# Performance work log

Hardware: AMD Instinct MI355X
Metric: run time of the kernel (lower is better)

The kernel has to match this reference:

```python
import jax, jax.numpy as jnp
import numpy as np
from jax import lax

B, T, C = 2, 2048, 1024
H, D = 16, 64            # num_heads, head_dim
K = 4                    # short conv kernel size
BASE = 10000.0
MAX_SEQ = 262144.0
ORIG_MAX = 8192.0
SCALING = 32.0
EPS = 1e-6


def _rope_cos_sin(t_len):
    ar = jnp.arange(0, D, 2).astype(jnp.float32) / D           # (D/2,)
    ext = MAX_SEQ / ORIG_MAX
    scaled_base = BASE * ext ** (D / (D - 2))
    inv_freq = 1.0 / scaled_base ** ar                          # (D/2,)
    freq_extra = 1.0 / BASE ** ar
    wavelen = 2 * np.pi / freq_extra
    beta_fast, beta_slow = 1.0, 32.0
    mscale = jnp.clip((wavelen - beta_fast) / (beta_slow - beta_fast), 0.0, 1.0)
    scale = 1.0 + (SCALING - 1.0) * mscale                      # per-freq t scaling
    t = jnp.arange(t_len, dtype=jnp.float32)[:, None] / scale[None, :]
    freqs = t * inv_freq[None, :]                               # (T, D/2)
    emb = jnp.concatenate([freqs, freqs], axis=-1)              # (T, D)
    return jnp.cos(emb), jnp.sin(emb)


def _apply_rotary(x, cos, sin):
    # x: (B,T,H,D); cos/sin: (T,D); faithful to torch interleaved indexing
    ce = cos[None, :, None, ::2]
    se = sin[None, :, None, ::2]
    x1, x2 = x[..., ::2], x[..., 1::2]
    return jnp.concatenate([x1 * ce - x2 * se, x1 * se + x2 * ce], axis=-1)


def _short_conv(x, w, b):
    # causal depthwise conv1d + silu. x: (B,T,C), w: (C,1,K), b: (C,)
    xp = jnp.pad(x, ((0, 0), (K - 1, 0), (0, 0))).transpose(0, 2, 1)  # (B,C,T+K-1)
    y = lax.conv_general_dilated(xp, w, window_strides=(1,), padding='VALID',
                                 feature_group_count=C,
                                 dimension_numbers=('NCH', 'OIH', 'NCH'))
    y = y + b[None, :, None]
    return jax.nn.silu(y.transpose(0, 2, 1))


def _l2norm(x):
    n = jnp.sqrt(jnp.sum(x * x, axis=-1, keepdims=True))
    return x / jnp.maximum(n, 1e-12)


def _rmsnorm(x, w):
    ms = jnp.mean(x.astype(jnp.float32) ** 2, axis=-1, keepdims=True).astype(x.dtype)
    return w * (x * lax.rsqrt(ms + EPS))


def setup_inputs() -> dict:
    key = jax.random.key(0)
    ks = jax.random.split(key, 20)
    s = 0.02
    inp = {
        'x': jax.random.normal(ks[0], (B, T, C), jnp.float32),
        'Wq': jax.random.normal(ks[1], (H * D, C), jnp.float32) * s,
        'Wk': jax.random.normal(ks[2], (H * D, C), jnp.float32) * s,
        'Wv': jax.random.normal(ks[3], (H * D, C), jnp.float32) * s,
        'Wg': jax.random.normal(ks[4], (H * D, C), jnp.float32) * s,
        'Wo': jax.random.normal(ks[5], (C, H * D), jnp.float32) * s,
        'Wb': jax.random.normal(ks[6], (H, C), jnp.float32) * s,
        'bb': jnp.zeros((H,), jnp.float32),
        'Wgk': jax.random.normal(ks[7], (H, C), jnp.float32) * s,
        'bgk': jnp.zeros((H,), jnp.float32),
        'conv_q_w': jax.random.normal(ks[8], (H * D, 1, K), jnp.float32) * 0.1,
        'conv_q_b': jnp.zeros((H * D,), jnp.float32),
        'conv_k_w': jax.random.normal(ks[9], (H * D, 1, K), jnp.float32) * 0.1,
        'conv_k_b': jnp.zeros((H * D,), jnp.float32),
        'conv_v_w': jax.random.normal(ks[10], (H * D, 1, K), jnp.float32) * 0.1,
        'conv_v_b': jnp.zeros((H * D,), jnp.float32),
        'A_log': jnp.log(jax.random.uniform(ks[11], (H,), jnp.float32, 1e-4, 16.0)),
        'Dp': jnp.ones((H,), jnp.float32),
        'dt_bias': jax.random.uniform(ks[12], (H,), jnp.float32, -0.01, 0.01),
        'o_norm_w': jnp.ones((D,), jnp.float32),
    }
    return inp


def reference(x, Wq, Wk, Wv, Wg, Wo, Wb, bb, Wgk, bgk,
              conv_q_w, conv_q_b, conv_k_w, conv_k_b, conv_v_w, conv_v_b,
              A_log, Dp, dt_bias, o_norm_w):
    q = _short_conv(x @ Wq.T, conv_q_w, conv_q_b)
    k = _short_conv(x @ Wk.T, conv_k_w, conv_k_b)
    v = _short_conv(x @ Wv.T, conv_v_w, conv_v_b)
    g = (x @ Wg.T).reshape(B, T, H, D)

    q = q.reshape(B, T, H, D)
    k = k.reshape(B, T, H, D)
    v = v.reshape(B, T, H, D)

    cos, sin = _rope_cos_sin(T)
    q = _l2norm(_apply_rotary(q, cos, sin))
    k = _l2norm(_apply_rotary(k, cos, sin))

    beta = jax.nn.sigmoid(x @ Wb.T + bb)                       # (B,T,H)
    gk = x @ Wgk.T + bgk                                       # (B,T,H)
    A = jnp.exp(A_log)
    alpha = jnp.exp(-A[None, None, :] * jax.nn.softplus(gk + dt_bias))  # (B,T,H)

    # gated delta rule: S_t = alpha_t*(S - beta_t*(S k)k^T) + beta_t*v k^T; o_t = S_t q_t
    def step(S, inp):
        qt, kt, vt, at, bt = inp                               # (B,H,D) x3, (B,H) x2
        Sk = jnp.einsum('bhvk,bhk->bhv', S, kt)
        outer = kt[:, :, None, :]
        S = (at[:, :, None, None] * (S - bt[:, :, None, None] * Sk[..., None] * outer)
             + bt[:, :, None, None] * vt[..., None] * outer)
        o = jnp.einsum('bhvk,bhk->bhv', S, qt)
        return S, o

    tm = lambda a: jnp.swapaxes(a, 0, 1)                        # time-major
    S0 = jnp.zeros((B, H, D, D), x.dtype)
    _, o = lax.scan(step, S0, (tm(q), tm(k), tm(v), tm(alpha), tm(beta)))
    o = jnp.swapaxes(o, 0, 1)                                  # (B,T,H,D)

    o = o + Dp[None, None, :, None] * v                        # D skip connection
    o = g * jax.nn.silu(_rmsnorm(o, o_norm_w))                 # fused RMSNorm-swish gate
    return o.reshape(B, T, H * D) @ Wo.T
```

## Files before the change

### kernel.cpp

```cpp
#include <hip/hip_runtime.h>

#define Bsz 2
#define Tsz 2048
#define Csz 1024
#define Hsz 16
#define Dsz 64
#define BT (Bsz*Tsz)

typedef unsigned short u16;
typedef __attribute__((ext_vector_type(8))) short bf16x8_t;
typedef __attribute__((ext_vector_type(4))) float f32x4;
typedef __attribute__((ext_vector_type(4))) unsigned short us4;

#define MF(a,b,c) __builtin_amdgcn_mfma_f32_16x16x32_bf16(a,b,c,0,0,0)

__device__ __forceinline__ float bf2f(u16 u){
    union { unsigned i; float f; } c; c.i = ((unsigned)u) << 16; return c.f;
}
__device__ __forceinline__ u16 f2bf(float f){
    union { float f; unsigned i; } c; c.f = f;
    unsigned i = c.i;
    unsigned r = (i + 0x7fffu + ((i >> 16) & 1u)) >> 16;
    return (u16)r;
}
__device__ __forceinline__ void gload_lds16(const void* g, void* l){
    __builtin_amdgcn_global_load_lds(
        (const __attribute__((address_space(1))) unsigned int*)g,
        (__attribute__((address_space(3))) unsigned int*)l, 16, 0, 0);
}

__global__ void rope_tables_k(float* __restrict__ ctab, float* __restrict__ stab){
    int idx = blockIdx.x * blockDim.x + threadIdx.x;
    if (idx >= Tsz * 16) return;
    int t = idx >> 4, m = idx & 15;
    float arf = (float)m / 16.f;
    double sb = 10000.0 * pow(32.0, 64.0 / 62.0);
    float invf = (float)(1.0 / pow(sb, (double)arf));
    float fe   = (float)(1.0 / pow(10000.0, (double)arf));
    float wl   = 6.283185307179586f / fe;
    float ms   = fminf(fmaxf((wl - 1.0f) / 31.0f, 0.f), 1.f);
    float scale = 1.f + 31.f * ms;
    float freq = ((float)t / scale) * invf;
    ctab[idx] = cosf(freq);
    stab[idx] = sinf(freq);
}

__global__ void cvt_f32_bf16_k(const float* __restrict__ in, u16* __restrict__ out, int n){
    int i = (blockIdx.x * blockDim.x + threadIdx.x) * 4;
    if (i >= n) return;
    float4 v = *(const float4*)(in + i);
    us4 o; o.x = f2bf(v.x); o.y = f2bf(v.y); o.z = f2bf(v.z); o.w = f2bf(v.w);
    *(us4*)(out + i) = o;
}

__global__ __launch_bounds__(256) void gemm_bf16_nt(
    const u16* __restrict__ A, const u16* __restrict__ Bw,
    float* __restrict__ Cf, u16* __restrict__ Cb,
    int gm, long sstride, int Kdim)
{
    __shared__ u16 As[2][128*32];
    __shared__ u16 Bs[2][128*32];

    const int nwg = gridDim.x;
    const int q8  = nwg >> 3;
    const int id  = blockIdx.x;
    const int swz = (id & 7) * q8 + (id >> 3);
    const int bx  = swz % gm;
    const int by  = swz / gm;

    const int tid = threadIdx.x;
    const int w  = tid >> 6, l = tid & 63;
    const int lm = l & 15,  lg = l >> 4;
    const int wm = (w >> 1) << 6;
    const int wn = (w & 1) << 6;

    const int r0  = (w << 4) + (l >> 2);
    const int kof = (l & 3) * 8;
    const long ga0 = (long)(bx * 128 + r0)      * Kdim + kof;
    const long ga1 = (long)(bx * 128 + r0 + 64) * Kdim + kof;
    const long gb0 = (long)(by * 128 + r0)      * Kdim + kof;
    const long gb1 = (long)(by * 128 + r0 + 64) * Kdim + kof;
    const int  ldst = r0 * 32 + kof;

    f32x4 acc[4][4];
#pragma unroll
    for (int i = 0; i < 4; i++)
#pragma unroll
        for (int j = 0; j < 4; j++) acc[i][j] = (f32x4){0.f, 0.f, 0.f, 0.f};

    const int nt = Kdim >> 5;
#define STAGE(B_, T_) do { int k0_ = (T_) << 5;                       \
        gload_lds16(A  + ga0 + k0_, &As[B_][ldst]);                   \
        gload_lds16(A  + ga1 + k0_, &As[B_][ldst + 2048]);            \
        gload_lds16(Bw + gb0 + k0_, &Bs[B_][ldst]);                   \
        gload_lds16(Bw + gb1 + k0_, &Bs[B_][ldst + 2048]);            \
    } while (0)

    STAGE(0, 0);
    __syncthreads();
    int buf = 0;
    for (int t = 0; t < nt; t++) {
        if (t + 1 < nt) STAGE(buf ^ 1, t + 1);
        bf16x8_t av[4], bv[4];
#pragma unroll
        for (int i = 0; i < 4; i++) av[i] = *(const bf16x8_t*)&As[buf][(wm + i*16 + lm)*32 + lg*8];
#pragma unroll
        for (int j = 0; j < 4; j++) bv[j] = *(const bf16x8_t*)&Bs[buf][(wn + j*16 + lm)*32 + lg*8];
#pragma unroll
        for (int i = 0; i < 4; i++)
#pragma unroll
            for (int j = 0; j < 4; j++)
                acc[i][j] = MF(av[i], bv[j], acc[i][j]);
        __syncthreads();
        buf ^= 1;
    }
#undef STAGE

    const int crow0 = bx * 128 + wm + lg * 4;
    const int ccol0 = by * 128 + wn + lm;
#pragma unroll
    for (int i = 0; i < 4; i++)
#pragma unroll
        for (int j = 0; j < 4; j++)
#pragma unroll
            for (int r = 0; r < 4; r++) {
                long row = crow0 + i * 16 + r;
                int  col = ccol0 + j * 16;
                float vv = acc[i][j][r];
                if (Cf) Cf[row * 1024 + col] = vv;
                else    Cb[(long)(col >> 10) * sstride + row * 1024 + (col & 1023)] = f2bf(vv);
            }
}

__global__ __launch_bounds__(256) void conv_silu_k(
    const u16* __restrict__ pre, const float* __restrict__ w,
    const float* __restrict__ bias, float* __restrict__ out)
{
    int c  = blockIdx.y * 256 + threadIdx.x;
    int bi = blockIdx.x;
    int b  = bi >> 5;
    int t0 = (bi & 31) << 6;
    float w0 = w[c*4+0], w1 = w[c*4+1], w2 = w[c*4+2], w3 = w[c*4+3];
    float bs = bias[c];
    long base = ((long)b * Tsz) * Csz + c;
    float xm3 = (t0 >= 3) ? bf2f(pre[base + (long)(t0-3)*Csz]) : 0.f;
    float xm2 = (t0 >= 2) ? bf2f(pre[base + (long)(t0-2)*Csz]) : 0.f;
    float xm1 = (t0 >= 1) ? bf2f(pre[base + (long)(t0-1)*Csz]) : 0.f;
    for (int t = t0; t < t0 + 64; t++) {
        float xc = bf2f(pre[base + (long)t * Csz]);
        float z  = bs + w0*xm3 + w1*xm2 + w2*xm1 + w3*xc;
        out[base + (long)t * Csz] = z / (1.f + expf(-z));
        xm3 = xm2; xm2 = xm1; xm1 = xc;
    }
}

__global__ __launch_bounds__(256) void rope_l2norm_k(
    float* __restrict__ qk, const float* __restrict__ ctab, const float* __restrict__ stab)
{
    int row = blockIdx.x * 4 + (threadIdx.x >> 6);
    int j   = threadIdx.x & 63;
    int t   = (row >> 4) & (Tsz - 1);
    int p   = j & 31, m = j & 15, hi = j >> 5;
    float2 xv = *(const float2*)(qk + (long)row * 64 + p * 2);
    float c = ctab[t * 16 + m], s = stab[t * 16 + m];
    float val = hi ? (xv.x * s + xv.y * c) : (xv.x * c - xv.y * s);
    float ss = val * val;
#pragma unroll
    for (int off = 1; off < 64; off <<= 1) ss += __shfl_xor(ss, off);
    float inv = 1.f / fmaxf(sqrtf(ss), 1e-12f);
    qk[(long)row * 64 + j] = val * inv;
}

__global__ __launch_bounds__(256) void ab_k(
    const float* __restrict__ x,
    const float* __restrict__ Wb,  const float* __restrict__ bb,
    const float* __restrict__ Wgk, const float* __restrict__ bgk,
    const float* __restrict__ A_log, const float* __restrict__ dtb,
    float* __restrict__ lalpha, float* __restrict__ beta)
{
    __shared__ float xr[1024];
    int bt = blockIdx.x;
    const float* xp = x + (long)bt * 1024;
#pragma unroll
    for (int i = 0; i < 4; i++) xr[threadIdx.x + i * 256] = xp[threadIdx.x + i * 256];
    __syncthreads();
    int wv = threadIdx.x >> 6, l = threadIdx.x & 63;
#pragma unroll
    for (int oo = 0; oo < 8; oo++) {
        int o = wv * 8 + oo;
        int h = o & 15;
        const float* wr = (o < 16 ? Wb : Wgk) + (long)h * 1024;
        float p = 0.f;
#pragma unroll
        for (int i = 0; i < 16; i++) p += wr[l + i * 64] * xr[l + i * 64];
        for (int off = 32; off; off >>= 1) p += __shfl_xor(p, off);
        if (l == 0) {
            if (o < 16) {
                beta[bt * 16 + h] = 1.f / (1.f + expf(-(p + bb[h])));
            } else {
                float gk = p + bgk[h] + dtb[h];
                float sp = gk > 0.f ? gk + log1pf(expf(-gk)) : log1pf(expf(gk));
                lalpha[bt * 16 + h] = -expf(A_log[h]) * sp;
            }
        }
    }
}

__global__ __launch_bounds__(256) void chunk_prep_k(
    const float* __restrict__ q, const float* __restrict__ k, const float* __restrict__ v,
    const float* __restrict__ lalpha, const float* __restrict__ beta,
    u16* __restrict__ Wg_, u16* __restrict__ Amat_, u16* __restrict__ Qg_,
    u16* __restrict__ KpT_, float* __restrict__ U_, float* __restrict__ gend_)
{
    __shared__ u16   Kb[64][72];
    __shared__ u16   Qb[64][72];
    __shared__ float Lm[64][68];
    __shared__ float WU[64][132];
    __shared__ float lgS[64];
    __shared__ float betaS[64];

    const int tile = blockIdx.x;
    const int bh = tile >> 5, n = tile & 31;
    const int b = bh >> 4, h = bh & 15;
    const int t0 = n << 6;
    const int tid = threadIdx.x;
    const int lane = tid & 63, wv = tid >> 6;
    const int lm = lane & 15, lg = lane >> 4;

    if (wv == 0) {
        long rix = ((long)(b * Tsz + t0 + lane)) * Hsz + h;
        float lgv = lalpha[rix];
#pragma unroll
        for (int off = 1; off < 64; off <<= 1) {
            float u = __shfl_up(lgv, off);
            if (lane >= off) lgv += u;
        }
        lgS[lane] = lgv;
        betaS[lane] = beta[rix];
    }
    {
        int row = tid >> 2, c0 = (tid & 3) << 4;
        long gb = ((long)(b * Tsz + t0 + row) * Hsz + h) << 6;
#pragma unroll
        for (int j = 0; j < 4; j++) {
            float4 kk = *(const float4*)(k + gb + c0 + 4*j);
            float4 qq = *(const float4*)(q + gb + c0 + 4*j);
            us4 kw, qw;
            kw.x=f2bf(kk.x); kw.y=f2bf(kk.y); kw.z=f2bf(kk.z); kw.w=f2bf(kk.w);
            qw.x=f2bf(qq.x); qw.y=f2bf(qq.y); qw.z=f2bf(qq.z); qw.w=f2bf(qq.w);
            *(us4*)&Kb[row][c0 + 4*j] = kw;
            *(us4*)&Qb[row][c0 + 4*j] = qw;
        }
    }
    __syncthreads();

    {
        const int ar = 16*wv + lm;
        bf16x8_t Ka0 = *(const bf16x8_t*)&Kb[ar][8*lg];
        bf16x8_t Ka1 = *(const bf16x8_t*)&Kb[ar][32 + 8*lg];
        bf16x8_t Qa0 = *(const bf16x8_t*)&Qb[ar][8*lg];
        bf16x8_t Qa1 = *(const bf16x8_t*)&Qb[ar][32 + 8*lg];
        f32x4 aKK[4], aQK[4];
#pragma unroll
        for (int nt=0; nt<4; nt++){ aKK[nt]=(f32x4){0,0,0,0}; aQK[nt]=(f32x4){0,0,0,0}; }
#pragma unroll
        for (int nt=0; nt<4; nt++){
            int br = 16*nt + lm;
            bf16x8_t B0 = *(const bf16x8_t*)&Kb[br][8*lg];
            bf16x8_t B1 = *(const bf16x8_t*)&Kb[br][32 + 8*lg];
            aKK[nt] = MF(Ka0, B0, aKK[nt]); aKK[nt] = MF(Ka1, B1, aKK[nt]);
            aQK[nt] = MF(Qa0, B0, aQK[nt]); aQK[nt] = MF(Qa1, B1, aQK[nt]);
        }
#pragma unroll
        for (int r=0; r<4; r++){
            int t = 16*wv + 4*lg + r;
            float lgt = lgS[t];
            float bt = betaS[t];
#pragma unroll
            for (int nt=0; nt<4; nt++){
                int s = 16*nt + lm;
                float ratio = expf(lgt - lgS[s]);
                Lm[t][s] = (s < t) ? bt * ratio * aKK[nt][r] : 0.f;
                Amat_[(long)tile*4096 + t*64 + s] = f2bf((s <= t) ? ratio * aQK[nt][r] : 0.f);
            }
        }
    }
    {
        int row = tid >> 2, qd = tid & 3;
        long gb = ((long)(b * Tsz + t0 + row) * Hsz + h) << 6;
        float bt = betaS[row];
        float gt = expf(lgS[row]);
        if (qd < 2) {
            int c0 = qd * 32;
            float bg = bt * gt;
#pragma unroll
            for (int j = 0; j < 8; j++) {
                float4 kk = *(const float4*)(k + gb + c0 + 4*j);
                WU[row][c0+4*j+0] = bg*kk.x; WU[row][c0+4*j+1] = bg*kk.y;
                WU[row][c0+4*j+2] = bg*kk.z; WU[row][c0+4*j+3] = bg*kk.w;
            }
        } else {
            int c0 = (qd - 2) * 32;
#pragma unroll
            for (int j = 0; j < 8; j++) {
                float4 vv = *(const float4*)(v + gb + c0 + 4*j);
                WU[row][64+c0+4*j+0] = bt*vv.x; WU[row][64+c0+4*j+1] = bt*vv.y;
                WU[row][64+c0+4*j+2] = bt*vv.z; WU[row][64+c0+4*j+3] = bt*vv.w;
            }
        }
    }
    __syncthreads();

    if (tid < 128) {
        float X[64];
        X[0] = WU[0][tid];
#pragma unroll
        for (int r = 1; r < 64; r++) {
            float a0 = 0.f, a1 = 0.f, a2 = 0.f, a3 = 0.f;
            const float4* L4 = (const float4*)&Lm[r][0];
#pragma unroll
            for (int j = 0; 4*j < r; j++) {
                float4 lv = L4[j];
                int s = 4*j;
                a0 += lv.x * X[s];
                if (s+1 < r) a1 += lv.y * X[s+1];
                if (s+2 < r) a2 += lv.z * X[s+2];
                if (s+3 < r) a3 += lv.w * X[s+3];
            }
            X[r] = WU[r][tid] - ((a0+a1)+(a2+a3));
        }
#pragma unroll
        for (int r = 0; r < 64; r++) WU[r][tid] = X[r];
    }
    __syncthreads();

    {
        int row = tid >> 2, c0 = (tid & 3) << 4;
        float gt  = expf(lgS[row]);
        float lge = lgS[63];
        long tb = (long)tile * 4096;
#pragma unroll
        for (int c = c0; c < c0 + 16; c++) {
            Wg_[tb + row*64 + c] = f2bf(WU[row][c]);
            U_ [tb + row*64 + c] = WU[row][64 + c];
            Qg_[tb + row*64 + c] = f2bf(gt * bf2f(Qb[row][c]));
            KpT_[tb + row*64 + c] = f2bf(expf(lge - lgS[c]) * bf2f(Kb[c][row]));
        }
        if (tid == 0) gend_[tile] = expf(lge);
    }
}

__global__ __launch_bounds__(256) void chunk_scan_k(
    const u16* __restrict__ Wg_, const u16* __restrict__ Amat_, const u16* __restrict__ Qg_,
    const u16* __restrict__ KpT_, const float* __restrict__ U_, const float* __restrict__ gend_,
    u16* __restrict__ oact)
{
    __shared__ float Sl[64][68];
    __shared__ u16   CT[64][72];
    const int bh = blockIdx.x, b = bh >> 4, h = bh & 15;
    const int tid = threadIdx.x, lane = tid & 63, wv = tid >> 6;
    const int lm = lane & 15, lg = lane >> 4;

    for (int i = tid; i < 64*68; i += 256) (&Sl[0][0])[i] = 0.f;
    __syncthreads();

    for (int n = 0; n < 32; n++) {
        const long tb = ((long)(bh*32 + n)) << 12;
        const int ar = 16*wv + lm;
        bf16x8_t Wa0 = *(const bf16x8_t*)(Wg_  + tb + ar*64 + 8*lg);
        bf16x8_t Wa1 = *(const bf16x8_t*)(Wg_  + tb + ar*64 + 32 + 8*lg);
        bf16x8_t Qa0 = *(const bf16x8_t*)(Qg_  + tb + ar*64 + 8*lg);
        bf16x8_t Qa1 = *(const bf16x8_t*)(Qg_  + tb + ar*64 + 32 + 8*lg);
        bf16x8_t Aa0 = *(const bf16x8_t*)(Amat_+ tb + ar*64 + 8*lg);
        bf16x8_t Aa1 = *(const bf16x8_t*)(Amat_+ tb + ar*64 + 32 + 8*lg);
        bf16x8_t Kp[4][2];
#pragma unroll
        for (int nt=0; nt<4; nt++)
#pragma unroll
            for (int sh=0; sh<2; sh++)
                Kp[nt][sh] = *(const bf16x8_t*)(KpT_ + tb + (16*nt+lm)*64 + 32*sh + 8*lg);
        float Uv[4][4];
#pragma unroll
        for (int nt=0; nt<4; nt++)
#pragma unroll
            for (int r=0; r<4; r++)
                Uv[nt][r] = U_[tb + (16*wv + 4*lg + r)*64 + 16*nt + lm];
        const float ge = gend_[bh*32 + n];

        bf16x8_t Shi[4][2], Slo[4][2];
#pragma unroll
        for (int nt=0; nt<4; nt++)
#pragma unroll
            for (int kh=0; kh<2; kh++){
                const float* sp = &Sl[16*nt + lm][32*kh + 8*lg];
                float4 aa = *(const float4*)sp;
                float4 bb = *(const float4*)(sp + 4);
                float xs[8] = {aa.x,aa.y,aa.z,aa.w,bb.x,bb.y,bb.z,bb.w};
#pragma unroll
                for (int j=0; j<8; j++){
                    u16 hv = f2bf(xs[j]);
                    Shi[nt][kh][j] = (short)hv;
                    Slo[nt][kh][j] = (short)f2bf(xs[j] - bf2f(hv));
                }
            }
        float Sa[4][4];
#pragma unroll
        for (int nt=0; nt<4; nt++)
#pragma unroll
            for (int r=0; r<4; r++)
                Sa[nt][r] = Sl[16*wv + 4*lg + r][16*nt + lm];

        f32x4 accP[4];
#pragma unroll
        for (int nt=0; nt<4; nt++){
            accP[nt] = (f32x4){0,0,0,0};
            accP[nt] = MF(Wa0, Shi[nt][0], accP[nt]);
            accP[nt] = MF(Wa0, Slo[nt][0], accP[nt]);
            accP[nt] = MF(Wa1, Shi[nt][1], accP[nt]);
            accP[nt] = MF(Wa1, Slo[nt][1], accP[nt]);
        }
#pragma unroll
        for (int nt=0; nt<4; nt++)
#pragma unroll
            for (int r=0; r<4; r++)
                CT[16*nt + lm][16*wv + 4*lg + r] = f2bf(Uv[nt][r] - accP[nt][r]);
        f32x4 accO[4];
#pragma unroll
        for (int nt=0; nt<4; nt++){
            accO[nt] = (f32x4){0,0,0,0};
            accO[nt] = MF(Qa0, Shi[nt][0], accO[nt]);
            accO[nt] = MF(Qa0, Slo[nt][0], accO[nt]);
            accO[nt] = MF(Qa1, Shi[nt][1], accO[nt]);
            accO[nt] = MF(Qa1, Slo[nt][1], accO[nt]);
        }
        __syncthreads();

#pragma unroll
        for (int nt=0; nt<4; nt++){
            bf16x8_t C0 = *(const bf16x8_t*)&CT[16*nt + lm][8*lg];
            bf16x8_t C1 = *(const bf16x8_t*)&CT[16*nt + lm][32 + 8*lg];
            accO[nt] = MF(Aa0, C0, accO[nt]);
            accO[nt] = MF(Aa1, C1, accO[nt]);
        }
        bf16x8_t CTa0 = *(const bf16x8_t*)&CT[16*wv + lm][8*lg];
        bf16x8_t CTa1 = *(const bf16x8_t*)&CT[16*wv + lm][32 + 8*lg];
        f32x4 accS[4];
#pragma unroll
        for (int nt=0; nt<4; nt++){
            accS[nt] = (f32x4){ge*Sa[nt][0], ge*Sa[nt][1], ge*Sa[nt][2], ge*Sa[nt][3]};
            accS[nt] = MF(CTa0, Kp[nt][0], accS[nt]);
            accS[nt] = MF(CTa1, Kp[nt][1], accS[nt]);
        }
#pragma unroll
        for (int nt=0; nt<4; nt++)
#pragma unroll
            for (int r=0; r<4; r++)
                Sl[16*wv + 4*lg + r][16*nt + lm] = accS[nt][r];
        const int trow = n*64 + 16*wv + 4*lg;
#pragma unroll
        for (int nt=0; nt<4; nt++)
#pragma unroll
            for (int r=0; r<4; r++)
                oact[(long)(b*Tsz + trow + r)*1024 + h*64 + 16*nt + lm] = f2bf(accO[nt][r]);
        __syncthreads();
    }
}

__global__ __launch_bounds__(256) void epi2_k(
    u16* __restrict__ o, const u16* __restrict__ g, const float* __restrict__ vc,
    const float* __restrict__ Dp, const float* __restrict__ onw)
{
    long row = (long)blockIdx.x * 4 + (threadIdx.x >> 6);
    int lane = threadIdx.x & 63;
    int h = (int)(row & 15);
    long idx = (row << 6) + lane;
    float ov = bf2f(o[idx]) + Dp[h] * vc[idx];
    float gv = bf2f(g[idx]);
    float ss = ov * ov;
#pragma unroll
    for (int off = 1; off < 64; off <<= 1) ss += __shfl_xor(ss, off);
    float r   = rsqrtf(ss * (1.f / 64.f) + 1e-6f);
    float on  = onw[lane] * (ov * r);
    float sil = on / (1.f + expf(-on));
    o[idx] = f2bf(gv * sil);
}

extern "C" void kernel_launch(void* const* d_in, const int* in_sizes, int n_in,
                              void* d_out, int out_size, void* d_ws, size_t ws_size,
                              hipStream_t stream)
{
    const float* x    = (const float*)d_in[0];
    const float* Wq   = (const float*)d_in[1];
    const float* Wk   = (const float*)d_in[2];
    const float* Wv   = (const float*)d_in[3];
    const float* Wg   = (const float*)d_in[4];
    const float* Wo   = (const float*)d_in[5];
    const float* Wb   = (const float*)d_in[6];
    const float* bb   = (const float*)d_in[7];
    const float* Wgk  = (const float*)d_in[8];
    const float* bgk  = (const float*)d_in[9];
    const float* cqw  = (const float*)d_in[10];
    const float* cqb  = (const float*)d_in[11];
    const float* ckw  = (const float*)d_in[12];
    const float* ckb  = (const float*)d_in[13];
    const float* cvw  = (const float*)d_in[14];
    const float* cvb  = (const float*)d_in[15];
    const float* A_log= (const float*)d_in[16];
    const float* Dp   = (const float*)d_in[17];
    const float* dtb  = (const float*)d_in[18];
    const float* onw  = (const float*)d_in[19];
    float* out = (float*)d_out;

    char* p = (char*)d_ws;
    auto alloc = [&](size_t bytes) -> char* {
        char* r = p; p += (bytes + 255) & ~(size_t)255; return r;
    };
    const size_t NBT = (size_t)BT * Csz;
    const size_t NTILE = (size_t)32 * 32;
    u16*   xbf   = (u16*)  alloc(NBT * 2);
    u16*   wcat  = (u16*)  alloc((size_t)4 * Csz * Csz * 2);
    u16*   Wobf  = (u16*)  alloc((size_t)Csz * Csz * 2);
    u16*   qkvg  = (u16*)  alloc((size_t)4 * NBT * 2);
    float* qconv = (float*)alloc(NBT * 4);
    float* kconv = (float*)alloc(NBT * 4);
    float* ctab  = (float*)alloc((size_t)Tsz * 16 * 4);
    float* stab  = (float*)alloc((size_t)Tsz * 16 * 4);
    float* lalpha= (float*)alloc((size_t)BT * Hsz * 4);
    float* beta  = (float*)alloc((size_t)BT * Hsz * 4);
    u16*   Wg_t  = (u16*)  alloc(NTILE * 4096 * 2);
    u16*   Amat_t= (u16*)  alloc(NTILE * 4096 * 2);
    u16*   Qg_t  = (u16*)  alloc(NTILE * 4096 * 2);
    u16*   KpT_t = (u16*)  alloc(NTILE * 4096 * 2);
    float* U_t   = (float*)alloc(NTILE * 4096 * 4);
    float* gend_t= (float*)alloc(NTILE * 4);

    u16* Wqbf = wcat;
    u16* Wkbf = wcat + (size_t)Csz * Csz;
    u16* Wvbf = wcat + (size_t)2 * Csz * Csz;
    u16* Wgbf = wcat + (size_t)3 * Csz * Csz;
    u16* qpre = qkvg;
    u16* vpre = qkvg + 2 * NBT;
    u16* gbf  = qkvg + 3 * NBT;
    float* vconv = (float*)qpre;
    u16*   oact  = (u16*)vpre;

    rope_tables_k<<<(Tsz * 16 + 255) / 256, 256, 0, stream>>>(ctab, stab);

    cvt_f32_bf16_k<<<(int)(NBT / 4 + 255) / 256, 256, 0, stream>>>(x,  xbf,  (int)NBT);
    cvt_f32_bf16_k<<<(Csz * Csz / 4 + 255) / 256, 256, 0, stream>>>(Wq, Wqbf, Csz * Csz);
    cvt_f32_bf16_k<<<(Csz * Csz / 4 + 255) / 256, 256, 0, stream>>>(Wk, Wkbf, Csz * Csz);
    cvt_f32_bf16_k<<<(Csz * Csz / 4 + 255) / 256, 256, 0, stream>>>(Wv, Wvbf, Csz * Csz);
    cvt_f32_bf16_k<<<(Csz * Csz / 4 + 255) / 256, 256, 0, stream>>>(Wg, Wgbf, Csz * Csz);
    cvt_f32_bf16_k<<<(Csz * Csz / 4 + 255) / 256, 256, 0, stream>>>(Wo, Wobf, Csz * Csz);

    gemm_bf16_nt<<<32 * 32, 256, 0, stream>>>(xbf, wcat, nullptr, qkvg, 32, (long)NBT, Csz);

    dim3 cgrid(Bsz * (Tsz / 64), Csz / 256);
    conv_silu_k<<<cgrid, 256, 0, stream>>>(qpre,            cqw, cqb, qconv);
    conv_silu_k<<<cgrid, 256, 0, stream>>>(qkvg + NBT,      ckw, ckb, kconv);
    conv_silu_k<<<cgrid, 256, 0, stream>>>(vpre,            cvw, cvb, vconv);

    rope_l2norm_k<<<(Bsz * Tsz * Hsz) / 4, 256, 0, stream>>>(qconv, ctab, stab);
    rope_l2norm_k<<<(Bsz * Tsz * Hsz) / 4, 256, 0, stream>>>(kconv, ctab, stab);

    ab_k<<<BT, 256, 0, stream>>>(x, Wb, bb, Wgk, bgk, A_log, dtb, lalpha, beta);

    chunk_prep_k<<<1024, 256, 0, stream>>>(qconv, kconv, vconv, lalpha, beta,
                                           Wg_t, Amat_t, Qg_t, KpT_t, U_t, gend_t);

    chunk_scan_k<<<Bsz * Hsz, 256, 0, stream>>>(Wg_t, Amat_t, Qg_t, KpT_t, U_t, gend_t, oact);

    epi2_k<<<(BT * Hsz) / 4, 256, 0, stream>>>(oact, gbf, vconv, Dp, onw);

    gemm_bf16_nt<<<32 * 8, 256, 0, stream>>>(oact, Wobf, out, nullptr, 32, 0L, Csz);

    (void)in_sizes; (void)n_in; (void)out_size; (void)ws_size;
}
```

Before: 448.1 us.

## Split chunk scan state across value-dim slices into single-wave blocks

```diff
diff --git a/kernel.cpp b/kernel.cpp
--- a/kernel.cpp
+++ b/kernel.cpp
@@ -350,118 +350,117 @@
     }
 }
 
-__global__ __launch_bounds__(256) void chunk_scan_k(
+__global__ __launch_bounds__(64) void chunk_scan_k(
     const u16* __restrict__ Wg_, const u16* __restrict__ Amat_, const u16* __restrict__ Qg_,
     const u16* __restrict__ KpT_, const float* __restrict__ U_, const float* __restrict__ gend_,
     u16* __restrict__ oact)
 {
-    __shared__ float Sl[64][68];
-    __shared__ u16   CT[64][72];
-    const int bh = blockIdx.x, b = bh >> 4, h = bh & 15;
-    const int tid = threadIdx.x, lane = tid & 63, wv = tid >> 6;
+    __shared__ float Sl[16][68];
+    __shared__ u16   CT[16][72];
+    const int bid = blockIdx.x;
+    const int sl = bid >> 5, bh = bid & 31;
+    const int b = bh >> 4, h = bh & 15;
+    const int dv0 = sl << 4;
+    const int lane = threadIdx.x;
     const int lm = lane & 15, lg = lane >> 4;
 
-    for (int i = tid; i < 64*68; i += 256) (&Sl[0][0])[i] = 0.f;
-    __syncthreads();
+    f32x4 Sacc0 = {0,0,0,0}, Sacc1 = {0,0,0,0}, Sacc2 = {0,0,0,0}, Sacc3 = {0,0,0,0};
 
     for (int n = 0; n < 32; n++) {
         const long tb = ((long)(bh*32 + n)) << 12;
-        const int ar = 16*wv + lm;
-        bf16x8_t Wa0 = *(const bf16x8_t*)(Wg_  + tb + ar*64 + 8*lg);
-        bf16x8_t Wa1 = *(const bf16x8_t*)(Wg_  + tb + ar*64 + 32 + 8*lg);
-        bf16x8_t Qa0 = *(const bf16x8_t*)(Qg_  + tb + ar*64 + 8*lg);
-        bf16x8_t Qa1 = *(const bf16x8_t*)(Qg_  + tb + ar*64 + 32 + 8*lg);
-        bf16x8_t Aa0 = *(const bf16x8_t*)(Amat_+ tb + ar*64 + 8*lg);
-        bf16x8_t Aa1 = *(const bf16x8_t*)(Amat_+ tb + ar*64 + 32 + 8*lg);
-        bf16x8_t Kp[4][2];
-#pragma unroll
-        for (int nt=0; nt<4; nt++)
-#pragma unroll
-            for (int sh=0; sh<2; sh++)
-                Kp[nt][sh] = *(const bf16x8_t*)(KpT_ + tb + (16*nt+lm)*64 + 32*sh + 8*lg);
+#pragma unroll
+        for (int r = 0; r < 4; r++) {
+            Sl[4*lg + r][ 0 + lm] = Sacc0[r];
+            Sl[4*lg + r][16 + lm] = Sacc1[r];
+            Sl[4*lg + r][32 + lm] = Sacc2[r];
+            Sl[4*lg + r][48 + lm] = Sacc3[r];
+        }
+        bf16x8_t Wa[4][2], Qa[4][2];
+#pragma unroll
+        for (int ti = 0; ti < 4; ti++)
+#pragma unroll
+            for (int kh = 0; kh < 2; kh++) {
+                Wa[ti][kh] = *(const bf16x8_t*)(Wg_ + tb + (16*ti + lm)*64 + 32*kh + 8*lg);
+                Qa[ti][kh] = *(const bf16x8_t*)(Qg_ + tb + (16*ti + lm)*64 + 32*kh + 8*lg);
+            }
         float Uv[4][4];
 #pragma unroll
-        for (int nt=0; nt<4; nt++)
-#pragma unroll
-            for (int r=0; r<4; r++)
-                Uv[nt][r] = U_[tb + (16*wv + 4*lg + r)*64 + 16*nt + lm];
+        for (int ti = 0; ti < 4; ti++)
+#pragma unroll
+            for (int r = 0; r < 4; r++)
+                Uv[ti][r] = U_[tb + (16*ti + 4*lg + r)*64 + dv0 + lm];
         const float ge = gend_[bh*32 + n];
-
-        bf16x8_t Shi[4][2], Slo[4][2];
-#pragma unroll
-        for (int nt=0; nt<4; nt++)
-#pragma unroll
-            for (int kh=0; kh<2; kh++){
-                const float* sp = &Sl[16*nt + lm][32*kh + 8*lg];
-                float4 aa = *(const float4*)sp;
-                float4 bb = *(const float4*)(sp + 4);
-                float xs[8] = {aa.x,aa.y,aa.z,aa.w,bb.x,bb.y,bb.z,bb.w};
-#pragma unroll
-                for (int j=0; j<8; j++){
-                    u16 hv = f2bf(xs[j]);
-                    Shi[nt][kh][j] = (short)hv;
-                    Slo[nt][kh][j] = (short)f2bf(xs[j] - bf2f(hv));
-                }
-            }
-        float Sa[4][4];
-#pragma unroll
-        for (int nt=0; nt<4; nt++)
-#pragma unroll
-            for (int r=0; r<4; r++)
-                Sa[nt][r] = Sl[16*wv + 4*lg + r][16*nt + lm];
-
+        __syncthreads();
+        bf16x8_t Shi[2], Slo[2];
+#pragma unroll
+        for (int kh = 0; kh < 2; kh++) {
+            const float* sp = &Sl[lm][32*kh + 8*lg];
+            float4 aa = *(const float4*)sp;
+            float4 bb = *(const float4*)(sp + 4);
+            float xs[8] = {aa.x,aa.y,aa.z,aa.w,bb.x,bb.y,bb.z,bb.w};
+#pragma unroll
+            for (int j = 0; j < 8; j++) {
+                u16 hv = f2bf(xs[j]);
+                Shi[kh][j] = (short)hv;
+                Slo[kh][j] = (short)f2bf(xs[j] - bf2f(hv));
+            }
+        }
         f32x4 accP[4];
 #pragma unroll
-        for (int nt=0; nt<4; nt++){
-            accP[nt] = (f32x4){0,0,0,0};
-            accP[nt] = MF(Wa0, Shi[nt][0], accP[nt]);
-            accP[nt] = MF(Wa0, Slo[nt][0], accP[nt]);
-            accP[nt] = MF(Wa1, Shi[nt][1], accP[nt]);
-            accP[nt] = MF(Wa1, Slo[nt][1], accP[nt]);
-        }
-#pragma unroll
-        for (int nt=0; nt<4; nt++)
-#pragma unroll
-            for (int r=0; r<4; r++)
-                CT[16*nt + lm][16*wv + 4*lg + r] = f2bf(Uv[nt][r] - accP[nt][r]);
+        for (int ti = 0; ti < 4; ti++) {
+            accP[ti] = (f32x4){0,0,0,0};
+            accP[ti] = MF(Wa[ti][0], Shi[0], accP[ti]);
+            accP[ti] = MF(Wa[ti][0], Slo[0], accP[ti]);
+            accP[ti] = MF(Wa[ti][1], Shi[1], accP[ti]);
+            accP[ti] = MF(Wa[ti][1], Slo[1], accP[ti]);
+        }
+#pragma unroll
+        for (int ti = 0; ti < 4; ti++)
+#pragma unroll
+            for (int r = 0; r < 4; r++)
+                CT[lm][16*ti + 4*lg + r] = f2bf(Uv[ti][r] - accP[ti][r]);
+        bf16x8_t Aa[4][2], Kp[4][2];
+#pragma unroll
+        for (int ti = 0; ti < 4; ti++)
+#pragma unroll
+            for (int sh = 0; sh < 2; sh++) {
+                Aa[ti][sh] = *(const bf16x8_t*)(Amat_ + tb + (16*ti + lm)*64 + 32*sh + 8*lg);
+                Kp[ti][sh] = *(const bf16x8_t*)(KpT_  + tb + (16*ti + lm)*64 + 32*sh + 8*lg);
+            }
         f32x4 accO[4];
 #pragma unroll
-        for (int nt=0; nt<4; nt++){
-            accO[nt] = (f32x4){0,0,0,0};
-            accO[nt] = MF(Qa0, Shi[nt][0], accO[nt]);
-            accO[nt] = MF(Qa0, Slo[nt][0], accO[nt]);
-            accO[nt] = MF(Qa1, Shi[nt][1], accO[nt]);
-            accO[nt] = MF(Qa1, Slo[nt][1], accO[nt]);
+        for (int ti = 0; ti < 4; ti++) {
+            accO[ti] = (f32x4){0,0,0,0};
+            accO[ti] = MF(Qa[ti][0], Shi[0], accO[ti]);
+            accO[ti] = MF(Qa[ti][0], Slo[0], accO[ti]);
+            accO[ti] = MF(Qa[ti][1], Shi[1], accO[ti]);
+            accO[ti] = MF(Qa[ti][1], Slo[1], accO[ti]);
         }
         __syncthreads();
-
-#pragma unroll
-        for (int nt=0; nt<4; nt++){
-            bf16x8_t C0 = *(const bf16x8_t*)&CT[16*nt + lm][8*lg];
-            bf16x8_t C1 = *(const bf16x8_t*)&CT[16*nt + lm][32 + 8*lg];
-            accO[nt] = MF(Aa0, C0, accO[nt]);
-            accO[nt] = MF(Aa1, C1, accO[nt]);
-        }
-        bf16x8_t CTa0 = *(const bf16x8_t*)&CT[16*wv + lm][8*lg];
-        bf16x8_t CTa1 = *(const bf16x8_t*)&CT[16*wv + lm][32 + 8*lg];
-        f32x4 accS[4];
-#pragma unroll
-        for (int nt=0; nt<4; nt++){
-            accS[nt] = (f32x4){ge*Sa[nt][0], ge*Sa[nt][1], ge*Sa[nt][2], ge*Sa[nt][3]};
-            accS[nt] = MF(CTa0, Kp[nt][0], accS[nt]);
-            accS[nt] = MF(CTa1, Kp[nt][1], accS[nt]);
-        }
-#pragma unroll
-        for (int nt=0; nt<4; nt++)
-#pragma unroll
-            for (int r=0; r<4; r++)
-                Sl[16*wv + 4*lg + r][16*nt + lm] = accS[nt][r];
-        const int trow = n*64 + 16*wv + 4*lg;
-#pragma unroll
-        for (int nt=0; nt<4; nt++)
-#pragma unroll
-            for (int r=0; r<4; r++)
-                oact[(long)(b*Tsz + trow + r)*1024 + h*64 + 16*nt + lm] = f2bf(accO[nt][r]);
+        bf16x8_t CTf[2];
+        CTf[0] = *(const bf16x8_t*)&CT[lm][8*lg];
+        CTf[1] = *(const bf16x8_t*)&CT[lm][32 + 8*lg];
+#pragma unroll
+        for (int ti = 0; ti < 4; ti++) {
+            accO[ti] = MF(Aa[ti][0], CTf[0], accO[ti]);
+            accO[ti] = MF(Aa[ti][1], CTf[1], accO[ti]);
+        }
+        f32x4 accS0, accS1, accS2, accS3;
+        accS0 = (f32x4){ge*Sacc0[0], ge*Sacc0[1], ge*Sacc0[2], ge*Sacc0[3]};
+        accS1 = (f32x4){ge*Sacc1[0], ge*Sacc1[1], ge*Sacc1[2], ge*Sacc1[3]};
+        accS2 = (f32x4){ge*Sacc2[0], ge*Sacc2[1], ge*Sacc2[2], ge*Sacc2[3]};
+        accS3 = (f32x4){ge*Sacc3[0], ge*Sacc3[1], ge*Sacc3[2], ge*Sacc3[3]};
+        accS0 = MF(CTf[0], Kp[0][0], accS0); accS0 = MF(CTf[1], Kp[0][1], accS0);
+        accS1 = MF(CTf[0], Kp[1][0], accS1); accS1 = MF(CTf[1], Kp[1][1], accS1);
+        accS2 = MF(CTf[0], Kp[2][0], accS2); accS2 = MF(CTf[1], Kp[2][1], accS2);
+        accS3 = MF(CTf[0], Kp[3][0], accS3); accS3 = MF(CTf[1], Kp[3][1], accS3);
+        Sacc0 = accS0; Sacc1 = accS1; Sacc2 = accS2; Sacc3 = accS3;
+        const int trow = n*64 + 4*lg;
+#pragma unroll
+        for (int ti = 0; ti < 4; ti++)
+#pragma unroll
+            for (int r = 0; r < 4; r++)
+                oact[(long)(b*Tsz + trow + 16*ti + r)*1024 + h*64 + dv0 + lm] = f2bf(accO[ti][r]);
         __syncthreads();
     }
 }
@@ -568,7 +567,7 @@
     chunk_prep_k<<<1024, 256, 0, stream>>>(qconv, kconv, vconv, lalpha, beta,
                                            Wg_t, Amat_t, Qg_t, KpT_t, U_t, gend_t);
 
-    chunk_scan_k<<<Bsz * Hsz, 256, 0, stream>>>(Wg_t, Amat_t, Qg_t, KpT_t, U_t, gend_t, oact);
+    chunk_scan_k<<<128, 64, 0, stream>>>(Wg_t, Amat_t, Qg_t, KpT_t, U_t, gend_t, oact);
 
     epi2_k<<<(BT * Hsz) / 4, 256, 0, stream>>>(oact, gbf, vconv, Dp, onw);
 
```

Measured after the change: 416.1 us. 7.1% less time.
